# Optimization experiments

Hardware: AMD Instinct MI355X
Metric: run time of the kernel (lower is better)

The kernel has to match this reference:

```python
import jax, jax.numpy as jnp
import numpy as np

B, T, D = 64, 2048, 256


def setup_inputs() -> dict:
    key = jax.random.key(0)
    k_x, k_len, k_w, k_b, k_a = jax.random.split(key, 5)
    xs = jax.random.normal(k_x, (B, T, D), dtype=jnp.float32)
    # ragged lengths -> prefix mask, mimicking per-sample slicing in the torch loop
    lens = jax.random.randint(k_len, (B,), T // 4, T + 1)
    mask = (jnp.arange(T)[None, :] < lens[:, None]).astype(jnp.int32)
    mask2 = jnp.ones((B, T), dtype=jnp.int32)  # unused by the module
    W = jax.random.normal(k_w, (D, D), dtype=jnp.float32) * (1.0 / np.sqrt(D))
    b = jax.random.normal(k_b, (D,), dtype=jnp.float32) * 0.01
    attn = jax.random.normal(k_a, (D,), dtype=jnp.float32)  # nn.Parameter(D,1) squeezed
    return {"xs": xs, "mask": mask, "mask2": mask2, "W": W, "b": b, "attn": attn}


def reference(xs, mask, mask2, W, b, attn):
    # h = tanh(Linear(x)); torch Linear: x @ W.T + b
    h = jnp.tanh(jnp.einsum("btd,ed->bte", xs, W) + b)          # [B,T,D]
    scores = jnp.einsum("btd,d->bt", h, attn)                    # [B,T]
    valid = mask.astype(bool)
    scores = jnp.where(valid, scores, -jnp.inf)                  # softmax over valid frames only
    w = jax.nn.softmax(scores, axis=1)[..., None]                # [B,T,1]
    mu = jnp.sum(xs * w, axis=1)                                 # [B,D]
    var = jnp.maximum(jnp.sum(xs * xs * w, axis=1) - mu * mu, 1e-5)
    return jnp.concatenate([mu, jnp.sqrt(var)], axis=1)          # [B,2D]
```

## Files before the change

kernel.cpp:

```cpp
#include <hip/hip_runtime.h>
#include <hip/hip_bf16.h>
#include <math.h>

#define PB 64
#define PT 2048
#define PD 256
#define PM (PB * PT)

typedef __bf16 bf16x8 __attribute__((ext_vector_type(8)));
typedef short  s16x8  __attribute__((ext_vector_type(8)));
typedef float  f32x4  __attribute__((ext_vector_type(4)));

__device__ __forceinline__ short rne_bf16(float x) {
    unsigned u = __builtin_bit_cast(unsigned, x);
    return (short)((u + 0x7fffu + ((u >> 16) & 1u)) >> 16);
}

__device__ __forceinline__ void split_bf16(float x, short& hi, short& lo) {
    unsigned u = __builtin_bit_cast(unsigned, x);
    hi = (short)(u >> 16);
    float hf = __builtin_bit_cast(float, u & 0xffff0000u);
    lo = rne_bf16(x - hf);
}

__global__ __launch_bounds__(256) void prep_kernel(
    const float* __restrict__ W, short* __restrict__ Whi, short* __restrict__ Wlo)
{
    const int idx = blockIdx.x * 256 + threadIdx.x;
    const int e = idx >> 8;
    const int k = idx & 255;
    short h, l;
    split_bf16(W[idx], h, l);
    const int flat = (((e >> 4) * 8 + (k >> 5)) * 64 + ((k & 31) >> 3) * 16 + (e & 15)) * 8 + (k & 7);
    Whi[flat] = h;
    Wlo[flat] = l;
}

#define SBM 64

__global__ __launch_bounds__(256, 4) void score_kernel(
    const float* __restrict__ xs, const short* __restrict__ Whi,
    const short* __restrict__ Wlo, const float* __restrict__ bias,
    const float* __restrict__ attn, float* __restrict__ scores)
{
    __shared__ short Ah[4 * 8 * 64 * 8];
    __shared__ float sred[4][64];

    const int tid = threadIdx.x;
    const int bm  = blockIdx.x * SBM;

#pragma unroll
    for (int p = 0; p < 8; ++p) {
        const int r  = p * 8 + (tid >> 5);
        const int kb = tid & 31;
        const float4 a0 = *(const float4*)&xs[(bm + r) * PD + kb * 8];
        const float4 a1 = *(const float4*)&xs[(bm + r) * PD + kb * 8 + 4];
        const float f[8] = {a0.x, a0.y, a0.z, a0.w, a1.x, a1.y, a1.z, a1.w};
        s16x8 h;
#pragma unroll
        for (int j = 0; j < 8; ++j) h[j] = rne_bf16(f[j]);
        const int mt = r >> 4, m_loc = r & 15;
        const int kt = kb >> 2, quad = kb & 3;
        const int msw = m_loc ^ (kb & 7);
        *(s16x8*)&Ah[(((mt * 8 + kt) * 64) + quad * 16 + msw) * 8] = h;
    }
    __syncthreads();

    const int lane = tid & 63;
    const int w    = tid >> 6;
    const int quad = lane >> 4;
    const int nl   = lane & 15;

    f32x4 acc[4][4] = {};

#pragma unroll 2
    for (int kt = 0; kt < 8; ++kt) {
        bf16x8 bh[4], bl[4];
#pragma unroll
        for (int n = 0; n < 4; ++n) {
            const int nt = w * 4 + n;
            const int bidx = ((nt * 8 + kt) * 64 + lane) * 8;
            bh[n] = *(const bf16x8*)&Whi[bidx];
            bl[n] = *(const bf16x8*)&Wlo[bidx];
        }
        s16x8 ah[4];
        const int msw = nl ^ ((kt * 4 + quad) & 7);
#pragma unroll
        for (int m = 0; m < 4; ++m)
            ah[m] = *(const s16x8*)&Ah[((m * 8 + kt) * 64 + quad * 16 + msw) * 8];
#pragma unroll
        for (int m = 0; m < 4; ++m) {
            const bf16x8 ahm = __builtin_bit_cast(bf16x8, ah[m]);
#pragma unroll
            for (int n = 0; n < 4; ++n) {
                acc[m][n] = __builtin_amdgcn_mfma_f32_16x16x32_bf16(ahm, bh[n], acc[m][n], 0, 0, 0);
                acc[m][n] = __builtin_amdgcn_mfma_f32_16x16x32_bf16(ahm, bl[n], acc[m][n], 0, 0, 0);
            }
        }
    }

    float bv[4], av[4];
#pragma unroll
    for (int n = 0; n < 4; ++n) {
        const int col = w * 64 + n * 16 + nl;
        bv[n] = bias[col];
        av[n] = attn[col];
    }
#pragma unroll
    for (int m = 0; m < 4; ++m) {
        float rs[4] = {0.f, 0.f, 0.f, 0.f};
#pragma unroll
        for (int n = 0; n < 4; ++n) {
#pragma unroll
            for (int r = 0; r < 4; ++r) {
                const float u  = acc[m][n][r] + bv[n];
                const float e2 = __expf(2.f * u);
                const float th = 1.f - 2.f * __builtin_amdgcn_rcpf(e2 + 1.f);
                rs[r] = fmaf(th, av[n], rs[r]);
            }
        }
#pragma unroll
        for (int off = 1; off < 16; off <<= 1) {
#pragma unroll
            for (int r = 0; r < 4; ++r) rs[r] += __shfl_xor(rs[r], off);
        }
        if (nl == 0) {
#pragma unroll
            for (int r = 0; r < 4; ++r) sred[w][m * 16 + quad * 4 + r] = rs[r];
        }
    }
    __syncthreads();
    if (tid < 64)
        scores[bm + tid] = sred[0][tid] + sred[1][tid] + sred[2][tid] + sred[3][tid];
}

__global__ __launch_bounds__(256) void softmax_kernel(
    const int* __restrict__ mask, float* __restrict__ sw)
{
    const int b    = blockIdx.x;
    const int tid  = threadIdx.x;
    const int lane = tid & 63;
    const int wv   = tid >> 6;
    __shared__ float wred[4];

    float s[8];
    int   v[8];
    float mx = -INFINITY;
#pragma unroll
    for (int i = 0; i < 8; ++i) {
        const int t = i * 256 + tid;
        s[i] = sw[b * PT + t];
        v[i] = mask[b * PT + t];
        if (v[i]) mx = fmaxf(mx, s[i]);
    }
#pragma unroll
    for (int off = 1; off < 64; off <<= 1) mx = fmaxf(mx, __shfl_xor(mx, off));
    if (lane == 0) wred[wv] = mx;
    __syncthreads();
    mx = fmaxf(fmaxf(wred[0], wred[1]), fmaxf(wred[2], wred[3]));
    __syncthreads();

    float p[8];
    float ls = 0.f;
#pragma unroll
    for (int i = 0; i < 8; ++i) {
        p[i] = v[i] ? __expf(s[i] - mx) : 0.f;
        ls += p[i];
    }
#pragma unroll
    for (int off = 1; off < 64; off <<= 1) ls += __shfl_xor(ls, off);
    if (lane == 0) wred[wv] = ls;
    __syncthreads();
    const float inv = 1.f / (wred[0] + wred[1] + wred[2] + wred[3]);
#pragma unroll
    for (int i = 0; i < 8; ++i) sw[b * PT + i * 256 + tid] = p[i] * inv;
}

__global__ __launch_bounds__(256) void moments_kernel(
    const float* __restrict__ xs, const float* __restrict__ w,
    float* __restrict__ part)
{
    const int chunk = blockIdx.x;
    const int b     = blockIdx.y;
    const int tid   = threadIdx.x;
    const int c     = tid & 63;
    const int tq    = tid >> 6;

    __shared__ float  lw[128];
    __shared__ float4 rmu[4][64];
    __shared__ float4 rm2[4][64];

    if (tid < 128) lw[tid] = w[b * PT + chunk * 128 + tid];
    __syncthreads();

    float4 mu = {0.f, 0.f, 0.f, 0.f};
    float4 m2 = {0.f, 0.f, 0.f, 0.f};
    for (int i = 0; i < 32; ++i) {
        const int tl = tq * 32 + i;
        const float wv = lw[tl];
        const float4 x = *(const float4*)&xs[(b * PT + chunk * 128 + tl) * PD + c * 4];
        mu.x = fmaf(wv, x.x, mu.x); mu.y = fmaf(wv, x.y, mu.y);
        mu.z = fmaf(wv, x.z, mu.z); mu.w = fmaf(wv, x.w, mu.w);
        m2.x = fmaf(wv * x.x, x.x, m2.x); m2.y = fmaf(wv * x.y, x.y, m2.y);
        m2.z = fmaf(wv * x.z, x.z, m2.z); m2.w = fmaf(wv * x.w, x.w, m2.w);
    }
    rmu[tq][c] = mu;
    rm2[tq][c] = m2;
    __syncthreads();

    if (tid < 64) {
        float4 smu = rmu[0][tid], sm2 = rm2[0][tid];
        for (int q = 1; q < 4; ++q) {
            const float4 a = rmu[q][tid], d = rm2[q][tid];
            smu.x += a.x; smu.y += a.y; smu.z += a.z; smu.w += a.w;
            sm2.x += d.x; sm2.y += d.y; sm2.z += d.z; sm2.w += d.w;
        }
        const int base = (b * 16 + chunk) * 512;
        *(float4*)&part[base + tid * 4]       = smu;
        *(float4*)&part[base + 256 + tid * 4] = sm2;
    }
}

__global__ __launch_bounds__(256) void finalize_kernel(
    const float* __restrict__ part, float* __restrict__ out)
{
    const int b = blockIdx.x;
    const int d = threadIdx.x;
    float m1 = 0.f, m2 = 0.f;
#pragma unroll
    for (int ch = 0; ch < 16; ++ch) {
        const int base = (b * 16 + ch) * 512;
        m1 += part[base + d];
        m2 += part[base + 256 + d];
    }
    const float var = fmaxf(m2 - m1 * m1, 1e-5f);
    out[b * 512 + d]       = m1;
    out[b * 512 + 256 + d] = sqrtf(var);
}

extern "C" void kernel_launch(void* const* d_in, const int* in_sizes, int n_in,
                              void* d_out, int out_size, void* d_ws, size_t ws_size,
                              hipStream_t stream) {
    const float* xs   = (const float*)d_in[0];
    const int*   mask = (const int*)d_in[1];
    const float* W    = (const float*)d_in[3];
    const float* bias = (const float*)d_in[4];
    const float* attn = (const float*)d_in[5];
    float* out = (float*)d_out;

    float* scores = (float*)d_ws;
    float* part   = scores + PB * PT;
    short* Whi    = (short*)(part + PB * 16 * 512);
    short* Wlo    = Whi + PD * PD;

    prep_kernel<<<PD * PD / 256, 256, 0, stream>>>(W, Whi, Wlo);
    score_kernel<<<PM / SBM, 256, 0, stream>>>(xs, Whi, Wlo, bias, attn, scores);
    softmax_kernel<<<PB, 256, 0, stream>>>(mask, scores);
    moments_kernel<<<dim3(16, PB), 256, 0, stream>>>(xs, scores, part);
    finalize_kernel<<<PB, 256, 0, stream>>>(part, out);
}
```

Baseline: 252.3 us.

## Make score kernel persistent over four tiles with register-prefetched double buffering

Each score block now handles four 64-row tiles and keeps two LDS buffers. The next tile's global loads are issued into registers while the current tile runs its MFMAs, so load latency is hidden instead of exposed at the start of every block. Launch bounds drop to 2 blocks per CU because the prefetch registers and the doubled LDS raise per-block resources. The moments loop also gets an unroll pragma.

```diff
diff --git a/kernel.cpp b/kernel.cpp
--- a/kernel.cpp
+++ b/kernel.cpp
@@ -37,68 +37,25 @@
 }
 
 #define SBM 64
-
-__global__ __launch_bounds__(256, 4) void score_kernel(
+#define STILES 4
+
+__global__ __launch_bounds__(256, 2) void score_kernel(
     const float* __restrict__ xs, const short* __restrict__ Whi,
     const short* __restrict__ Wlo, const float* __restrict__ bias,
     const float* __restrict__ attn, float* __restrict__ scores)
 {
-    __shared__ short Ah[4 * 8 * 64 * 8];
+    __shared__ short Ah[2][4 * 8 * 64 * 8];
     __shared__ float sred[4][64];
 
     const int tid = threadIdx.x;
-    const int bm  = blockIdx.x * SBM;
-
-#pragma unroll
-    for (int p = 0; p < 8; ++p) {
-        const int r  = p * 8 + (tid >> 5);
-        const int kb = tid & 31;
-        const float4 a0 = *(const float4*)&xs[(bm + r) * PD + kb * 8];
-        const float4 a1 = *(const float4*)&xs[(bm + r) * PD + kb * 8 + 4];
-        const float f[8] = {a0.x, a0.y, a0.z, a0.w, a1.x, a1.y, a1.z, a1.w};
-        s16x8 h;
-#pragma unroll
-        for (int j = 0; j < 8; ++j) h[j] = rne_bf16(f[j]);
-        const int mt = r >> 4, m_loc = r & 15;
-        const int kt = kb >> 2, quad = kb & 3;
-        const int msw = m_loc ^ (kb & 7);
-        *(s16x8*)&Ah[(((mt * 8 + kt) * 64) + quad * 16 + msw) * 8] = h;
-    }
-    __syncthreads();
+    const int rr  = tid >> 5;
+    const int kb  = tid & 31;
 
     const int lane = tid & 63;
     const int w    = tid >> 6;
     const int quad = lane >> 4;
     const int nl   = lane & 15;
 
-    f32x4 acc[4][4] = {};
-
-#pragma unroll 2
-    for (int kt = 0; kt < 8; ++kt) {
-        bf16x8 bh[4], bl[4];
-#pragma unroll
-        for (int n = 0; n < 4; ++n) {
-            const int nt = w * 4 + n;
-            const int bidx = ((nt * 8 + kt) * 64 + lane) * 8;
-            bh[n] = *(const bf16x8*)&Whi[bidx];
-            bl[n] = *(const bf16x8*)&Wlo[bidx];
-        }
-        s16x8 ah[4];
-        const int msw = nl ^ ((kt * 4 + quad) & 7);
-#pragma unroll
-        for (int m = 0; m < 4; ++m)
-            ah[m] = *(const s16x8*)&Ah[((m * 8 + kt) * 64 + quad * 16 + msw) * 8];
-#pragma unroll
-        for (int m = 0; m < 4; ++m) {
-            const bf16x8 ahm = __builtin_bit_cast(bf16x8, ah[m]);
-#pragma unroll
-            for (int n = 0; n < 4; ++n) {
-                acc[m][n] = __builtin_amdgcn_mfma_f32_16x16x32_bf16(ahm, bh[n], acc[m][n], 0, 0, 0);
-                acc[m][n] = __builtin_amdgcn_mfma_f32_16x16x32_bf16(ahm, bl[n], acc[m][n], 0, 0, 0);
-            }
-        }
-    }
-
     float bv[4], av[4];
 #pragma unroll
     for (int n = 0; n < 4; ++n) {
@@ -106,32 +63,104 @@
         bv[n] = bias[col];
         av[n] = attn[col];
     }
-#pragma unroll
-    for (int m = 0; m < 4; ++m) {
-        float rs[4] = {0.f, 0.f, 0.f, 0.f};
-#pragma unroll
-        for (int n = 0; n < 4; ++n) {
-#pragma unroll
-            for (int r = 0; r < 4; ++r) {
-                const float u  = acc[m][n][r] + bv[n];
-                const float e2 = __expf(2.f * u);
-                const float th = 1.f - 2.f * __builtin_amdgcn_rcpf(e2 + 1.f);
-                rs[r] = fmaf(th, av[n], rs[r]);
-            }
-        }
-#pragma unroll
-        for (int off = 1; off < 16; off <<= 1) {
-#pragma unroll
-            for (int r = 0; r < 4; ++r) rs[r] += __shfl_xor(rs[r], off);
-        }
-        if (nl == 0) {
-#pragma unroll
-            for (int r = 0; r < 4; ++r) sred[w][m * 16 + quad * 4 + r] = rs[r];
-        }
-    }
-    __syncthreads();
-    if (tid < 64)
-        scores[bm + tid] = sred[0][tid] + sred[1][tid] + sred[2][tid] + sred[3][tid];
+
+    const int tile0 = blockIdx.x * STILES;
+    float4 ra[8], rb[8];
+
+    auto issue = [&](int tile) {
+        const float* src = xs + (size_t)tile * SBM * PD;
+#pragma unroll
+        for (int p = 0; p < 8; ++p) {
+            const int r = p * 8 + rr;
+            ra[p] = *(const float4*)&src[r * PD + kb * 8];
+            rb[p] = *(const float4*)&src[r * PD + kb * 8 + 4];
+        }
+    };
+    auto convert_store = [&](int buf) {
+#pragma unroll
+        for (int p = 0; p < 8; ++p) {
+            const int r = p * 8 + rr;
+            const float f[8] = {ra[p].x, ra[p].y, ra[p].z, ra[p].w,
+                                rb[p].x, rb[p].y, rb[p].z, rb[p].w};
+            s16x8 h;
+#pragma unroll
+            for (int j = 0; j < 8; ++j) h[j] = rne_bf16(f[j]);
+            const int mt = r >> 4, m_loc = r & 15;
+            const int kt = kb >> 2, q = kb & 3;
+            const int msw = m_loc ^ (kb & 7);
+            *(s16x8*)&Ah[buf][(((mt * 8 + kt) * 64) + q * 16 + msw) * 8] = h;
+        }
+    };
+
+    issue(tile0);
+    convert_store(0);
+    issue(tile0 + 1);
+    __syncthreads();
+
+    for (int t = 0; t < STILES; ++t) {
+        const int buf = t & 1;
+        f32x4 acc[4][4] = {};
+
+#pragma unroll 2
+        for (int kt = 0; kt < 8; ++kt) {
+            bf16x8 bh[4], bl[4];
+#pragma unroll
+            for (int n = 0; n < 4; ++n) {
+                const int nt = w * 4 + n;
+                const int bidx = ((nt * 8 + kt) * 64 + lane) * 8;
+                bh[n] = *(const bf16x8*)&Whi[bidx];
+                bl[n] = *(const bf16x8*)&Wlo[bidx];
+            }
+            s16x8 ah[4];
+            const int msw = nl ^ ((kt * 4 + quad) & 7);
+#pragma unroll
+            for (int m = 0; m < 4; ++m)
+                ah[m] = *(const s16x8*)&Ah[buf][((m * 8 + kt) * 64 + quad * 16 + msw) * 8];
+#pragma unroll
+            for (int m = 0; m < 4; ++m) {
+                const bf16x8 ahm = __builtin_bit_cast(bf16x8, ah[m]);
+#pragma unroll
+                for (int n = 0; n < 4; ++n) {
+                    acc[m][n] = __builtin_amdgcn_mfma_f32_16x16x32_bf16(ahm, bh[n], acc[m][n], 0, 0, 0);
+                    acc[m][n] = __builtin_amdgcn_mfma_f32_16x16x32_bf16(ahm, bl[n], acc[m][n], 0, 0, 0);
+                }
+            }
+        }
+
+#pragma unroll
+        for (int m = 0; m < 4; ++m) {
+            float rs[4] = {0.f, 0.f, 0.f, 0.f};
+#pragma unroll
+            for (int n = 0; n < 4; ++n) {
+#pragma unroll
+                for (int r = 0; r < 4; ++r) {
+                    const float u  = acc[m][n][r] + bv[n];
+                    const float e2 = __expf(2.f * u);
+                    const float th = 1.f - 2.f * __builtin_amdgcn_rcpf(e2 + 1.f);
+                    rs[r] = fmaf(th, av[n], rs[r]);
+                }
+            }
+#pragma unroll
+            for (int off = 1; off < 16; off <<= 1) {
+#pragma unroll
+                for (int r = 0; r < 4; ++r) rs[r] += __shfl_xor(rs[r], off);
+            }
+            if (nl == 0) {
+#pragma unroll
+                for (int r = 0; r < 4; ++r) sred[w][m * 16 + quad * 4 + r] = rs[r];
+            }
+        }
+        __syncthreads();
+        if (tid < 64)
+            scores[(tile0 + t) * SBM + tid] =
+                sred[0][tid] + sred[1][tid] + sred[2][tid] + sred[3][tid];
+
+        if (t < STILES - 1) {
+            convert_store(buf ^ 1);
+            if (t < STILES - 2) issue(tile0 + t + 2);
+        }
+        __syncthreads();
+    }
 }
 
 __global__ __launch_bounds__(256) void softmax_kernel(
@@ -195,6 +224,7 @@
 
     float4 mu = {0.f, 0.f, 0.f, 0.f};
     float4 m2 = {0.f, 0.f, 0.f, 0.f};
+#pragma unroll 8
     for (int i = 0; i < 32; ++i) {
         const int tl = tq * 32 + i;
         const float wv = lw[tl];
@@ -254,7 +284,7 @@
     short* Wlo    = Whi + PD * PD;
 
     prep_kernel<<<PD * PD / 256, 256, 0, stream>>>(W, Whi, Wlo);
-    score_kernel<<<PM / SBM, 256, 0, stream>>>(xs, Whi, Wlo, bias, attn, scores);
+    score_kernel<<<PM / (SBM * STILES), 256, 0, stream>>>(xs, Whi, Wlo, bias, attn, scores);
     softmax_kernel<<<PB, 256, 0, stream>>>(mask, scores);
     moments_kernel<<<dim3(16, PB), 256, 0, stream>>>(xs, scores, part);
     finalize_kernel<<<PB, 256, 0, stream>>>(part, out);
```

Result: no change. 256.7 us (+1.7%).
